# Kernel optimization log

Hardware: AMD Instinct MI355X
Metric: run time of the kernel (lower is better)

Reference implementation:

```python
import jax, jax.numpy as jnp
import numpy as np

LN_EPS = 1e-5
DEG_EPS = 1e-6
H = 256
N_VAR = 100000
NUM_CON = 50000
E = 300000


def setup_inputs() -> dict:
    key = jax.random.key(0)
    ks = jax.random.split(key, 8)
    s = 1.0 / np.sqrt(H)
    s2 = 1.0 / np.sqrt(H + 1)
    return {
        "x_var": jax.random.normal(ks[0], (N_VAR, H), dtype=jnp.float32),
        "src": jax.random.randint(ks[1], (E,), 0, N_VAR, dtype=jnp.int32),
        "dst": jax.random.randint(ks[2], (E,), 0, NUM_CON, dtype=jnp.int32),
        "clue_values": jax.random.normal(ks[3], (NUM_CON,), dtype=jnp.float32),
        "num_con": NUM_CON,
        "msg_W": jax.random.uniform(ks[4], (H, H), jnp.float32, -s, s),
        "msg_b": jax.random.uniform(ks[5], (H,), jnp.float32, -s, s),
        "update_W": jax.random.uniform(ks[6], (H, H + 1), jnp.float32, -s2, s2),
        "update_b": jax.random.uniform(ks[7], (H,), jnp.float32, -s2, s2),
        "ln_w": jnp.ones((H,), jnp.float32),
        "ln_b": jnp.zeros((H,), jnp.float32),
    }


def reference(x_var, src, dst, clue_values, num_con, msg_W, msg_b, update_W, update_b, ln_w, ln_b):
    # gather + linear message transform: (E, H)
    msgs = x_var[src] @ msg_W.T + msg_b
    # degree-normalized scatter-add into constraints: (num_con, H)
    agg = jax.ops.segment_sum(msgs, dst, num_segments=num_con)
    deg = jax.ops.segment_sum(jnp.ones((dst.shape[0],), msgs.dtype), dst, num_segments=num_con)
    agg = agg / (deg[:, None] + DEG_EPS)
    # concat clue scalar, update MLP, ReLU
    h = jnp.concatenate([agg, clue_values[:, None]], axis=1)
    out = jax.nn.relu(h @ update_W.T + update_b)
    # LayerNorm over last dim
    mu = out.mean(axis=-1, keepdims=True)
    var = out.var(axis=-1, keepdims=True)
    return (out - mu) * jax.lax.rsqrt(var + LN_EPS) * ln_w + ln_b
```

## Files before the change

### kernel.cpp

```cpp
#include <hip/hip_runtime.h>

#define HD 256
#define LN_EPS 1e-5f
#define DEG_EPS 1e-6f
#define CAP 64

typedef __attribute__((ext_vector_type(8))) short short8;
typedef __attribute__((ext_vector_type(4))) short s16x4;
typedef __attribute__((ext_vector_type(4))) float f32x4;
typedef __attribute__((ext_vector_type(4))) int i32x4;

__device__ inline unsigned short f2bf(float f) {
    union { float f; unsigned int u; } v; v.f = f;
    unsigned int r = v.u + 0x7FFFu + ((v.u >> 16) & 1u);
    return (unsigned short)(r >> 16);
}
__device__ inline float bf2f(unsigned short h) {
    union { unsigned int u; float f; } v; v.u = ((unsigned int)h) << 16;
    return v.f;
}
__device__ inline short8 cvt8(float4 u0, float4 u1) {
    short8 o;
    o[0] = (short)f2bf(u0.x); o[1] = (short)f2bf(u0.y);
    o[2] = (short)f2bf(u0.z); o[3] = (short)f2bf(u0.w);
    o[4] = (short)f2bf(u1.x); o[5] = (short)f2bf(u1.y);
    o[6] = (short)f2bf(u1.z); o[7] = (short)f2bf(u1.w);
    return o;
}

__global__ __launch_bounds__(256) void prep0_kernel(
    int* __restrict__ counts, int num_con,
    const float* __restrict__ msg_W, const float* __restrict__ msg_b,
    const float* __restrict__ upd_W,
    unsigned short* __restrict__ w12b, float* __restrict__ bv,
    float* __restrict__ ucol, int zb) {
    int b = blockIdx.x, tid = threadIdx.x;
    if (b < zb) {
        int i = (b * 256 + tid) * 4;
        if (i + 4 <= num_con) *(i32x4*)(counts + i) = (i32x4){0, 0, 0, 0};
        else for (; i < num_con; ++i) counts[i] = 0;
    } else {
        int j = b - zb, k = tid;
        float a0 = 0.f, a1 = 0.f, a2 = 0.f, a3 = 0.f, accb = 0.f;
#pragma unroll 2
        for (int m = 0; m < 256; m += 4) {
            float w0 = upd_W[j * 257 + m + 0];
            float w1 = upd_W[j * 257 + m + 1];
            float w2 = upd_W[j * 257 + m + 2];
            float w3 = upd_W[j * 257 + m + 3];
            a0 = fmaf(w0, msg_W[(m + 0) * 256 + k], a0);
            a1 = fmaf(w1, msg_W[(m + 1) * 256 + k], a1);
            a2 = fmaf(w2, msg_W[(m + 2) * 256 + k], a2);
            a3 = fmaf(w3, msg_W[(m + 3) * 256 + k], a3);
            accb = fmaf(w0, msg_b[m + 0], accb);
            accb = fmaf(w1, msg_b[m + 1], accb);
            accb = fmaf(w2, msg_b[m + 2], accb);
            accb = fmaf(w3, msg_b[m + 3], accb);
        }
        w12b[j * 256 + k] = f2bf((a0 + a1) + (a2 + a3));
        if (k == 0) { bv[j] = accb; ucol[j] = upd_W[j * 257 + 256]; }
    }
}

__global__ __launch_bounds__(256) void fill_kernel(
    const int* __restrict__ src, const int* __restrict__ dst,
    int* __restrict__ counts, int* __restrict__ eidx, int E) {
    int e = blockIdx.x * 256 + threadIdx.x;
    if (e >= E) return;
    int d = dst[e];
    int p = atomicAdd(&counts[d], 1);
    if (p < CAP) eidx[d * CAP + p] = src[e];
}

__global__ __launch_bounds__(256) void ygemm_kernel(
    const float* __restrict__ x, const unsigned short* __restrict__ w12b,
    unsigned short* __restrict__ y, int n_var, int ntiles) {

    __shared__ unsigned short sA[2][16 * 256];
    const int tid = threadIdx.x, w = tid >> 6, lane = tid & 63;
    const int lr = lane & 15, lg = lane >> 4;

    short8 bfr[4][8];
#pragma unroll
    for (int jt = 0; jt < 4; ++jt)
#pragma unroll
        for (int ks = 0; ks < 8; ++ks)
            bfr[jt][ks] = *(const short8*)(w12b + (w * 64 + jt * 16 + lr) * HD + lg * 8 + ks * 32);

    const int srow = tid >> 4, scol = (tid & 15) * 16;

    int buf = 0;
#pragma unroll 1
    for (int rt = blockIdx.x; rt < ntiles; rt += gridDim.x) {
        int r0 = rt * 16;
        {
            int arc = min(r0 + srow, n_var - 1);
            const float* gp = x + (long)arc * HD + scol;
            float4 u0 = *(const float4*)(gp);
            float4 u1 = *(const float4*)(gp + 4);
            float4 u2 = *(const float4*)(gp + 8);
            float4 u3 = *(const float4*)(gp + 12);
            int b0 = (srow * 512 + scol * 2) ^ ((srow & 7) << 4);
            int b1 = (srow * 512 + scol * 2 + 16) ^ ((srow & 7) << 4);
            *(short8*)((char*)&sA[buf][0] + b0) = cvt8(u0, u1);
            *(short8*)((char*)&sA[buf][0] + b1) = cvt8(u2, u3);
        }
        __syncthreads();

        short8 af[8];
#pragma unroll
        for (int ks = 0; ks < 8; ++ks) {
            int byte = (lr * 512 + (ks * 32 + lg * 8) * 2) ^ ((lr & 7) << 4);
            af[ks] = *(const short8*)((char*)&sA[buf][0] + byte);
        }

        f32x4 acc[4] = {{0.f,0.f,0.f,0.f},{0.f,0.f,0.f,0.f},{0.f,0.f,0.f,0.f},{0.f,0.f,0.f,0.f}};
#pragma unroll
        for (int ks = 0; ks < 8; ++ks)
#pragma unroll
            for (int jt = 0; jt < 4; ++jt)
                acc[jt] = __builtin_amdgcn_mfma_f32_16x16x32_bf16(af[ks], bfr[jt][ks], acc[jt], 0, 0, 0);

#pragma unroll
        for (int q = 0; q < 4; ++q) {
            int grow = r0 + lg * 4 + q;
            if (grow < n_var) {
                s16x4 o;
#pragma unroll
                for (int jt = 0; jt < 4; ++jt) o[jt] = (short)f2bf(acc[jt][q]);
                *(s16x4*)(y + (long)grow * HD + w * 64 + lr * 4) = o;
            }
        }
        buf ^= 1;
    }
}

__global__ __launch_bounds__(256) void gatherln_kernel(
    const unsigned short* __restrict__ y, const int* __restrict__ counts,
    const int* __restrict__ eidx, const float* __restrict__ clue,
    const float* __restrict__ bv, const float* __restrict__ ucol,
    const float* __restrict__ upd_b,
    const float* __restrict__ ln_w, const float* __restrict__ ln_b,
    float* __restrict__ out, int num_con) {
    int row  = blockIdx.x * 4 + (threadIdx.x >> 6);
    int lane = threadIdx.x & 63;
    if (row >= num_con) return;
    int cnt = counts[row];
    int cgo = min(cnt, CAP);
    int sid = (lane < cgo) ? eidx[row * CAP + lane] : 0;
    float a0 = 0.f, a1 = 0.f, a2 = 0.f, a3 = 0.f;
#pragma unroll 1
    for (int i = 0; i < cgo; i += 8) {
        int s[8];
#pragma unroll
        for (int u = 0; u < 8; ++u) s[u] = __shfl(sid, i + u, 64);
        s16x4 v[8];
#pragma unroll
        for (int u = 0; u < 8; ++u)
            v[u] = *(const s16x4*)(y + (long)s[u] * HD + lane * 4);
#pragma unroll
        for (int u = 0; u < 8; ++u) {
            float wg = (i + u < cgo) ? 1.f : 0.f;
            a0 = fmaf(bf2f((unsigned short)v[u][0]), wg, a0);
            a1 = fmaf(bf2f((unsigned short)v[u][1]), wg, a1);
            a2 = fmaf(bf2f((unsigned short)v[u][2]), wg, a2);
            a3 = fmaf(bf2f((unsigned short)v[u][3]), wg, a3);
        }
    }
    int c0 = ((lane >> 4) << 6) + (lane & 15);
    float sc = 1.0f / ((float)cnt + DEG_EPS);
    float tc = (float)cnt * sc;
    float cl = clue[row];
    float z[4] = {a0, a1, a2, a3};
    float s = 0.f, s2 = 0.f;
#pragma unroll
    for (int jt = 0; jt < 4; ++jt) {
        int c = c0 + jt * 16;
        float zz = fmaxf(z[jt] * sc + tc * bv[c] + cl * ucol[c] + upd_b[c], 0.0f);
        z[jt] = zz;
        s += zz; s2 += zz * zz;
    }
#pragma unroll
    for (int m = 1; m < 64; m <<= 1) {
        s  += __shfl_xor(s,  m, 64);
        s2 += __shfl_xor(s2, m, 64);
    }
    float mu = s * (1.0f / HD);
    float var = s2 * (1.0f / HD) - mu * mu;
    float rs = rsqrtf(var + LN_EPS);
    float* gp = out + (long)row * HD;
#pragma unroll
    for (int jt = 0; jt < 4; ++jt) {
        int c = c0 + jt * 16;
        gp[c] = (z[jt] - mu) * rs * ln_w[c] + ln_b[c];
    }
}

extern "C" void kernel_launch(void* const* d_in, const int* in_sizes, int n_in,
                              void* d_out, int out_size, void* d_ws, size_t ws_size,
                              hipStream_t stream) {
    const float* x_var = (const float*)d_in[0];
    const int*   src   = (const int*)d_in[1];
    const int*   dst   = (const int*)d_in[2];
    const float* clue  = (const float*)d_in[3];
    const float* msg_W = (const float*)d_in[5];
    const float* msg_b = (const float*)d_in[6];
    const float* upd_W = (const float*)d_in[7];
    const float* upd_b = (const float*)d_in[8];
    const float* ln_w  = (const float*)d_in[9];
    const float* ln_b  = (const float*)d_in[10];

    int E = in_sizes[1];
    long n_x = in_sizes[0];
    int n_var = (int)(n_x / HD);
    int num_con = out_size / HD;
    int ntiles_v = (n_var + 15) / 16;

    char* ws = (char*)d_ws;
    int* counts = (int*)ws;
    int* eidx   = (int*)(ws + (((size_t)num_con * 4 + 255) & ~(size_t)255));
    char* after = (char*)(eidx + (size_t)num_con * CAP);
    size_t yoff = ((size_t)(after - ws) + 255) & ~(size_t)255;
    unsigned short* yv = (unsigned short*)(ws + yoff);
    size_t woff = (yoff + (size_t)n_var * HD * 2 + 255) & ~(size_t)255;
    unsigned short* w12b = (unsigned short*)(ws + woff);
    float* bvp  = (float*)(w12b + 256 * 256);
    float* ucol = bvp + 256;

    int zb = (num_con + 1023) / 1024;
    prep0_kernel<<<zb + 256, 256, 0, stream>>>(
        counts, num_con, msg_W, msg_b, upd_W, w12b, bvp, ucol, zb);

    fill_kernel<<<(E + 255) / 256, 256, 0, stream>>>(src, dst, counts, eidx, E);

    ygemm_kernel<<<2048, 256, 0, stream>>>(x_var, w12b, yv, n_var, ntiles_v);

    gatherln_kernel<<<(num_con + 3) / 4, 256, 0, stream>>>(
        yv, counts, eidx, clue, bvp, ucol, upd_b, ln_w, ln_b,
        (float*)d_out, num_con);
}
```

Before: 111.4 us.

## Fuse edge fill into GEMM launch and load A fragments directly from global

Merges the edge-bucketing fill kernel and the Y GEMM kernel into one launch, with the first block range doing the atomic fill and the remaining blocks doing the GEMM. This removes a launch and lets the two independent phases overlap. The GEMM also drops the LDS staging and __syncthreads: each lane loads its own A fragment from global, converts it to bf16 and feeds the MFMAs, in two half-K batches to limit register pressure. The cost is less coalesced global loads (each lane reads 32-byte chunks spread across rows) and possibly higher register use.

Measured after the change: 142.8 us. 1.28x slower.

```diff
diff --git a/kernel.cpp b/kernel.cpp
--- a/kernel.cpp
+++ b/kernel.cpp
@@ -62,22 +62,24 @@
     }
 }
 
-__global__ __launch_bounds__(256) void fill_kernel(
+__global__ __launch_bounds__(256) void fillygemm_kernel(
     const int* __restrict__ src, const int* __restrict__ dst,
-    int* __restrict__ counts, int* __restrict__ eidx, int E) {
-    int e = blockIdx.x * 256 + threadIdx.x;
-    if (e >= E) return;
-    int d = dst[e];
-    int p = atomicAdd(&counts[d], 1);
-    if (p < CAP) eidx[d * CAP + p] = src[e];
-}
-
-__global__ __launch_bounds__(256) void ygemm_kernel(
+    int* __restrict__ counts, int* __restrict__ eidx, int E, int FB,
     const float* __restrict__ x, const unsigned short* __restrict__ w12b,
-    unsigned short* __restrict__ y, int n_var, int ntiles) {
-
-    __shared__ unsigned short sA[2][16 * 256];
-    const int tid = threadIdx.x, w = tid >> 6, lane = tid & 63;
+    unsigned short* __restrict__ y, int n_var, int ntiles, int NG) {
+
+    const int tid = threadIdx.x;
+    if ((int)blockIdx.x < FB) {
+        int e = blockIdx.x * 256 + tid;
+        if (e < E) {
+            int d = dst[e];
+            int p = atomicAdd(&counts[d], 1);
+            if (p < CAP) eidx[d * CAP + p] = src[e];
+        }
+        return;
+    }
+
+    const int wv = tid >> 6, lane = tid & 63;
     const int lr = lane & 15, lg = lane >> 4;
 
     short8 bfr[4][8];
@@ -85,41 +87,46 @@
     for (int jt = 0; jt < 4; ++jt)
 #pragma unroll
         for (int ks = 0; ks < 8; ++ks)
-            bfr[jt][ks] = *(const short8*)(w12b + (w * 64 + jt * 16 + lr) * HD + lg * 8 + ks * 32);
-
-    const int srow = tid >> 4, scol = (tid & 15) * 16;
-
-    int buf = 0;
+            bfr[jt][ks] = *(const short8*)(w12b + (wv * 64 + jt * 16 + lr) * HD + lg * 8 + ks * 32);
+
 #pragma unroll 1
-    for (int rt = blockIdx.x; rt < ntiles; rt += gridDim.x) {
+    for (int rt = (int)blockIdx.x - FB; rt < ntiles; rt += NG) {
         int r0 = rt * 16;
+        int arow = min(r0 + lr, n_var - 1);
+        const float* ap = x + (long)arow * HD + lg * 8;
+
+        f32x4 acc[4] = {{0.f,0.f,0.f,0.f},{0.f,0.f,0.f,0.f},{0.f,0.f,0.f,0.f},{0.f,0.f,0.f,0.f}};
+
         {
-            int arc = min(r0 + srow, n_var - 1);
-            const float* gp = x + (long)arc * HD + scol;
-            float4 u0 = *(const float4*)(gp);
-            float4 u1 = *(const float4*)(gp + 4);
-            float4 u2 = *(const float4*)(gp + 8);
-            float4 u3 = *(const float4*)(gp + 12);
-            int b0 = (srow * 512 + scol * 2) ^ ((srow & 7) << 4);
-            int b1 = (srow * 512 + scol * 2 + 16) ^ ((srow & 7) << 4);
-            *(short8*)((char*)&sA[buf][0] + b0) = cvt8(u0, u1);
-            *(short8*)((char*)&sA[buf][0] + b1) = cvt8(u2, u3);
-        }
-        __syncthreads();
-
-        short8 af[8];
-#pragma unroll
-        for (int ks = 0; ks < 8; ++ks) {
-            int byte = (lr * 512 + (ks * 32 + lg * 8) * 2) ^ ((lr & 7) << 4);
-            af[ks] = *(const short8*)((char*)&sA[buf][0] + byte);
-        }
-
-        f32x4 acc[4] = {{0.f,0.f,0.f,0.f},{0.f,0.f,0.f,0.f},{0.f,0.f,0.f,0.f},{0.f,0.f,0.f,0.f}};
-#pragma unroll
-        for (int ks = 0; ks < 8; ++ks)
-#pragma unroll
-            for (int jt = 0; jt < 4; ++jt)
-                acc[jt] = __builtin_amdgcn_mfma_f32_16x16x32_bf16(af[ks], bfr[jt][ks], acc[jt], 0, 0, 0);
+            float4 t[8];
+#pragma unroll
+            for (int ks = 0; ks < 4; ++ks) {
+                t[2 * ks]     = *(const float4*)(ap + ks * 32);
+                t[2 * ks + 1] = *(const float4*)(ap + ks * 32 + 4);
+            }
+#pragma unroll
+            for (int ks = 0; ks < 4; ++ks) {
+                short8 af = cvt8(t[2 * ks], t[2 * ks + 1]);
+#pragma unroll
+                for (int jt = 0; jt < 4; ++jt)
+                    acc[jt] = __builtin_amdgcn_mfma_f32_16x16x32_bf16(af, bfr[jt][ks], acc[jt], 0, 0, 0);
+            }
+        }
+        {
+            float4 t[8];
+#pragma unroll
+            for (int ks = 4; ks < 8; ++ks) {
+                t[2 * (ks - 4)]     = *(const float4*)(ap + ks * 32);
+                t[2 * (ks - 4) + 1] = *(const float4*)(ap + ks * 32 + 4);
+            }
+#pragma unroll
+            for (int ks = 4; ks < 8; ++ks) {
+                short8 af = cvt8(t[2 * (ks - 4)], t[2 * (ks - 4) + 1]);
+#pragma unroll
+                for (int jt = 0; jt < 4; ++jt)
+                    acc[jt] = __builtin_amdgcn_mfma_f32_16x16x32_bf16(af, bfr[jt][ks], acc[jt], 0, 0, 0);
+            }
+        }
 
 #pragma unroll
         for (int q = 0; q < 4; ++q) {
@@ -128,10 +135,9 @@
                 s16x4 o;
 #pragma unroll
                 for (int jt = 0; jt < 4; ++jt) o[jt] = (short)f2bf(acc[jt][q]);
-                *(s16x4*)(y + (long)grow * HD + w * 64 + lr * 4) = o;
-            }
-        }
-        buf ^= 1;
+                *(s16x4*)(y + (long)grow * HD + wv * 64 + lr * 4) = o;
+            }
+        }
     }
 }
 
@@ -231,9 +237,11 @@
     prep0_kernel<<<zb + 256, 256, 0, stream>>>(
         counts, num_con, msg_W, msg_b, upd_W, w12b, bvp, ucol, zb);
 
-    fill_kernel<<<(E + 255) / 256, 256, 0, stream>>>(src, dst, counts, eidx, E);
-
-    ygemm_kernel<<<2048, 256, 0, stream>>>(x_var, w12b, yv, n_var, ntiles_v);
+    int FB = (E + 255) / 256;
+    int NG = 2048;
+    fillygemm_kernel<<<FB + NG, 256, 0, stream>>>(
+        src, dst, counts, eidx, E, FB,
+        x_var, w12b, yv, n_var, ntiles_v, NG);
 
     gatherln_kernel<<<(num_con + 3) / 4, 256, 0, stream>>>(
         yv, counts, eidx, clue, bvp, ucol, upd_b, ln_w, ln_b,
```
